# Kernel tuning notes

Measured on AMD Instinct MI355X. Metric: run time of the kernel, lower is better.

Reference implementation:

```python
import jax, jax.numpy as jnp
import numpy as np

B, CI, CO, A = 2048, 32, 32, 16   # batch, caps_in, caps_out, atom
ITER_NUM = 5


def setup_inputs() -> dict:
    key = jax.random.key(0)
    k1, = jax.random.split(key, 1)
    x = jax.random.normal(k1, (B, CI, CO, A), dtype=jnp.float32)
    gamma = jnp.ones((1, CI, 1, A), dtype=jnp.float32)
    beta = jnp.zeros((1, CI, 1, A), dtype=jnp.float32)
    return {"x": x, "gamma": gamma, "beta": beta}


def _iter_norm_inv_sqrt(sigma, iter_num):
    # sigma: [CI, A, A] batched covariance; Newton-Schulz inverse square root.
    a = sigma.shape[-1]
    trace = jnp.trace(sigma, axis1=-2, axis2=-1)[:, None, None]  # [CI,1,1]
    sigma_n = sigma / trace                                      # trace-normalize
    p = jnp.broadcast_to(jnp.eye(a, dtype=sigma.dtype), sigma.shape)
    for _ in range(iter_num):
        p = 0.5 * (3.0 * p - p @ p @ p @ sigma_n)
    return p / jnp.sqrt(trace)


def reference(x, gamma, beta):
    b, ci, co, a = x.shape
    # center over batch and caps_out axes (axes [0, 2])
    mean = jnp.mean(x, axis=(0, 2), keepdims=True)                # [1,CI,1,A]
    centered = x - mean
    # [CI, B*CO, A]
    c = jnp.transpose(centered, (1, 0, 2, 3)).reshape(ci, b * co, a)
    # per-capsule covariance, normalized by (batch*caps_out - 1)
    sigma = jnp.einsum('cna,cnb->cab', c, c) / (jnp.float32(b * co) - 1.0)
    w = _iter_norm_inv_sqrt(sigma, ITER_NUM)                       # [CI,A,A]
    dec = jnp.einsum('cna,cab->cnb', c, w)                         # whiten
    dec = jnp.transpose(dec.reshape(ci, b, co, a), (1, 0, 2, 3))   # [B,CI,CO,A]
    return dec * gamma + beta
```

## Files before the change

kernel.cpp:

```cpp
#include <hip/hip_runtime.h>
#include <hip/hip_bf16.h>
#include <math.h>

constexpr int CI = 32;
constexpr int CO = 32;
constexpr float INV_N   = 1.0f / 65536.0f;
constexpr float INV_NM1 = 1.0f / 65535.0f;

constexpr int NCHUNK = 32;
constexpr int PART_STRIDE = 272;

constexpr int WS_PART = 0;
constexpr int WS_WG   = CI * NCHUNK * PART_STRIDE;
constexpr int WS_C0   = WS_WG + CI * 256;

constexpr int BSTRIDE = 16384;

using f32x4  = __attribute__((ext_vector_type(4))) float;
using bf16x8 = __attribute__((ext_vector_type(8))) short;

__global__ __launch_bounds__(256) void k_stats(const float* __restrict__ x,
                                               float* __restrict__ ws) {
    const int ci    = blockIdx.x & 31;
    const int chunk = blockIdx.x >> 5;
    const int tid   = threadIdx.x;
    const int lane  = tid & 63;
    const int wv    = tid >> 6;
    const int m     = lane & 15;
    const int g     = lane >> 4;

    f32x4 acc = {0.0f, 0.0f, 0.0f, 0.0f};
    float sacc = 0.0f;

    const int b0 = chunk * 64 + wv * 16;
    const float* p = x + ((size_t)(b0 * 32 + ci) * 32 + g * 8) * 16 + m;

    float bA[8], bB[8], bC[8], bD[8];

    auto ld = [&](float (&d)[8], const float* q) {
#pragma unroll
        for (int j = 0; j < 8; ++j) d[j] = q[j * 16];
    };
    auto step = [&](float (&buf)[8]) {
        union { bf16x8 v; unsigned short h[8]; } fu;
#pragma unroll
        for (int j = 0; j < 8; ++j) {
            sacc += buf[j];
            fu.h[j] = __bfloat16_as_ushort(__float2bfloat16(buf[j]));
        }
        acc = __builtin_amdgcn_mfma_f32_16x16x32_bf16(fu.v, fu.v, acc, 0, 0, 0);
    };

    ld(bA, p);
    ld(bB, p + BSTRIDE);
    ld(bC, p + 2 * BSTRIDE);
    ld(bD, p + 3 * BSTRIDE);
    p += 4 * BSTRIDE;
#pragma unroll
    for (int rr = 0; rr < 4; ++rr) {
        step(bA); if (rr < 3) ld(bA, p);
        step(bB); if (rr < 3) ld(bB, p + BSTRIDE);
        step(bC); if (rr < 3) ld(bC, p + 2 * BSTRIDE);
        step(bD); if (rr < 3) { ld(bD, p + 3 * BSTRIDE); p += 4 * BSTRIDE; }
    }

    sacc += __shfl_xor(sacc, 16, 64);
    sacc += __shfl_xor(sacc, 32, 64);

    __shared__ float red[4][272];
#pragma unroll
    for (int q = 0; q < 4; ++q)
        red[wv][(g * 4 + q) * 17 + m] = acc[q];
    if (g == 0) red[wv][m * 17 + 16] = sacc;
    __syncthreads();

    float* slot = ws + WS_PART + (ci * NCHUNK + chunk) * PART_STRIDE;
    for (int e = tid; e < 272; e += 256)
        slot[e] = red[0][e] + red[1][e] + red[2][e] + red[3][e];
}

__global__ __launch_bounds__(256) void k_ns(const float* __restrict__ gamma,
                                            const float* __restrict__ beta,
                                            float* __restrict__ ws) {
    const int ci  = blockIdx.x;
    const int tid = threadIdx.x;
    const int r = tid >> 4, c = tid & 15;

    __shared__ float red2[272];
    __shared__ float sig[16][17];
    __shared__ float pm[16][17];
    __shared__ float t1[16][17];
    __shared__ float t2[16][17];
    __shared__ float trace_s;

    const float* base = ws + WS_PART + (size_t)ci * NCHUNK * PART_STRIDE;
    for (int e = tid; e < 272; e += 256) {
        float s = 0.0f;
#pragma unroll
        for (int ch = 0; ch < NCHUNK; ++ch)
            s += base[ch * PART_STRIDE + e];
        red2[e] = s;
    }
    __syncthreads();

    const float P_rc = red2[r * 17 + c];
    const float S_r  = red2[r * 17 + 16];
    const float S_c  = red2[c * 17 + 16];
    sig[r][c] = (P_rc - S_r * S_c * INV_N) * INV_NM1;
    __syncthreads();

    if (tid == 0) {
        float tr = 0.0f;
        for (int i = 0; i < 16; ++i) tr += sig[i][i];
        trace_s = tr;
    }
    __syncthreads();
    const float tr = trace_s;

    sig[r][c] = sig[r][c] / tr;
    pm[r][c]  = (r == c) ? 1.0f : 0.0f;
    __syncthreads();

    for (int it = 0; it < 5; ++it) {
        float a = 0.0f;
        for (int k = 0; k < 16; ++k) a += pm[r][k] * pm[k][c];
        t1[r][c] = a;
        __syncthreads();
        float b2 = 0.0f;
        for (int k = 0; k < 16; ++k) b2 += t1[r][k] * pm[k][c];
        t2[r][c] = b2;
        __syncthreads();
        float d = 0.0f;
        for (int k = 0; k < 16; ++k) d += t2[r][k] * sig[k][c];
        const float np = 0.5f * (3.0f * pm[r][c] - d);
        __syncthreads();
        pm[r][c] = np;
        __syncthreads();
    }

    const float inv_sqrt_tr = 1.0f / sqrtf(tr);
    const float gc = gamma[ci * 16 + c];
    ws[WS_WG + ci * 256 + r * 16 + c] = pm[r][c] * inv_sqrt_tr * gc;
    if (r == 0) {
        float s = 0.0f;
        for (int a = 0; a < 16; ++a) {
            const float mean_a = red2[a * 17 + 16] * INV_N;
            s += mean_a * pm[a][c];
        }
        ws[WS_C0 + ci * 16 + c] = beta[ci * 16 + c] - gc * s * inv_sqrt_tr;
    }
}

__global__ __launch_bounds__(256) void k_apply(const float* __restrict__ x,
                                               const float* __restrict__ ws,
                                               float* __restrict__ out) {
    const int ci    = blockIdx.x & 31;
    const int chunk = blockIdx.x >> 5;
    const int tid   = threadIdx.x;
    const int sub   = tid & 3;
    const int quad  = tid >> 2;
    const int b0    = sub * 4;

    float wg[16][4];
    const float* WG = ws + WS_WG + ci * 256;
#pragma unroll
    for (int a = 0; a < 16; ++a) {
        const float4 w4 = *reinterpret_cast<const float4*>(WG + a * 16 + b0);
        wg[a][0] = w4.x; wg[a][1] = w4.y; wg[a][2] = w4.z; wg[a][3] = w4.w;
    }
    const float4 c4 = *reinterpret_cast<const float4*>(ws + WS_C0 + ci * 16 + b0);
    const float c0[4] = {c4.x, c4.y, c4.z, c4.w};

    const size_t base =
        (((size_t)(chunk * 64 + (quad >> 5)) * 32 + ci) * 32 + (quad & 31)) * 16;
    const float* p = x + base;
    float* q = out + base + b0;

    auto body = [&](const float4& f0, const float4& f1,
                    const float4& f2, const float4& f3, float* qq) {
        const float v[16] = {f0.x, f0.y, f0.z, f0.w,  f1.x, f1.y, f1.z, f1.w,
                             f2.x, f2.y, f2.z, f2.w,  f3.x, f3.y, f3.z, f3.w};
        float oacc[4] = {c0[0], c0[1], c0[2], c0[3]};
#pragma unroll
        for (int a = 0; a < 16; ++a) {
#pragma unroll
            for (int i = 0; i < 4; ++i) oacc[i] += v[a] * wg[a][i];
        }
        f32x4 o;
        o.x = oacc[0]; o.y = oacc[1]; o.z = oacc[2]; o.w = oacc[3];
        __builtin_nontemporal_store(o, reinterpret_cast<f32x4*>(qq));
    };

    float4 f0 = *reinterpret_cast<const float4*>(p);
    float4 f1 = *reinterpret_cast<const float4*>(p + 4);
    float4 f2 = *reinterpret_cast<const float4*>(p + 8);
    float4 f3 = *reinterpret_cast<const float4*>(p + 12);

    for (int it = 0; it < 31; ++it) {
        const float* pn = p + 32768;
        const float4 g0 = *reinterpret_cast<const float4*>(pn);
        const float4 g1 = *reinterpret_cast<const float4*>(pn + 4);
        const float4 g2 = *reinterpret_cast<const float4*>(pn + 8);
        const float4 g3 = *reinterpret_cast<const float4*>(pn + 12);

        body(f0, f1, f2, f3, q);

        f0 = g0; f1 = g1; f2 = g2; f3 = g3;
        p = pn; q += 32768;
    }
    body(f0, f1, f2, f3, q);
}

extern "C" void kernel_launch(void* const* d_in, const int* in_sizes, int n_in,
                              void* d_out, int out_size, void* d_ws, size_t ws_size,
                              hipStream_t stream) {
    const float* x     = (const float*)d_in[0];
    const float* gamma = (const float*)d_in[1];
    const float* beta  = (const float*)d_in[2];
    float* out = (float*)d_out;
    float* ws  = (float*)d_ws;

    k_stats<<<dim3(1024), dim3(256), 0, stream>>>(x, ws);
    k_ns<<<dim3(32), dim3(256), 0, stream>>>(gamma, beta, ws);
    k_apply<<<dim3(1024), dim3(256), 0, stream>>>(x, ws, out);
}
```

Measured before the change: 76.04 us.

## Remap stats blocks to contiguous spans over 8 capsules, add reduction stage

Each k_stats block now covers 8 batch rows across 8 consecutive input capsules instead of 64 strided batches for a single capsule. Each wave reads contiguous 4 KB blocks and keeps 8 MFMA accumulators. Because partials grow to 256 spans per capsule, a new k_red kernel pre-reduces them into 8 per capsule before k_ns. The new layout should give more sequential DRAM access, at the cost of an extra launch, more partial-sum traffic, and higher register and LDS use per block.

```diff
diff --git a/kernel.cpp b/kernel.cpp
--- a/kernel.cpp
+++ b/kernel.cpp
@@ -7,76 +7,100 @@
 constexpr float INV_N   = 1.0f / 65536.0f;
 constexpr float INV_NM1 = 1.0f / 65535.0f;
 
-constexpr int NCHUNK = 32;
+constexpr int NSPAN = 256;
 constexpr int PART_STRIDE = 272;
-
 constexpr int WS_PART = 0;
-constexpr int WS_WG   = CI * NCHUNK * PART_STRIDE;
+constexpr int WS_MID  = CI * NSPAN * PART_STRIDE;
+constexpr int WS_WG   = WS_MID + CI * 8 * PART_STRIDE;
 constexpr int WS_C0   = WS_WG + CI * 256;
-
-constexpr int BSTRIDE = 16384;
 
 using f32x4  = __attribute__((ext_vector_type(4))) float;
 using bf16x8 = __attribute__((ext_vector_type(8))) short;
 
 __global__ __launch_bounds__(256) void k_stats(const float* __restrict__ x,
                                                float* __restrict__ ws) {
-    const int ci    = blockIdx.x & 31;
-    const int chunk = blockIdx.x >> 5;
-    const int tid   = threadIdx.x;
-    const int lane  = tid & 63;
-    const int wv    = tid >> 6;
-    const int m     = lane & 15;
-    const int g     = lane >> 4;
-
-    f32x4 acc = {0.0f, 0.0f, 0.0f, 0.0f};
-    float sacc = 0.0f;
-
-    const int b0 = chunk * 64 + wv * 16;
-    const float* p = x + ((size_t)(b0 * 32 + ci) * 32 + g * 8) * 16 + m;
-
-    float bA[8], bB[8], bC[8], bD[8];
-
+    const int cig  = blockIdx.x & 3;
+    const int span = blockIdx.x >> 2;
+    const int tid  = threadIdx.x;
+    const int lane = tid & 63;
+    const int wv   = tid >> 6;
+    const int m    = lane & 15;
+    const int g    = lane >> 4;
+
+    f32x4 acc[8];
+    float sacc[8];
+#pragma unroll
+    for (int l = 0; l < 8; ++l) {
+        acc[l] = f32x4{0.0f, 0.0f, 0.0f, 0.0f};
+        sacc[l] = 0.0f;
+    }
+
+    const float* pb = x +
+        (((size_t)(span * 8 + wv * 2) * 32 + cig * 8) * 32 + g * 8) * 16 + m;
+
+    float bufA[8], bufB[8];
     auto ld = [&](float (&d)[8], const float* q) {
 #pragma unroll
         for (int j = 0; j < 8; ++j) d[j] = q[j * 16];
     };
-    auto step = [&](float (&buf)[8]) {
+    auto step = [&](float (&buf)[8], int l) {
         union { bf16x8 v; unsigned short h[8]; } fu;
 #pragma unroll
         for (int j = 0; j < 8; ++j) {
-            sacc += buf[j];
+            sacc[l] += buf[j];
             fu.h[j] = __bfloat16_as_ushort(__float2bfloat16(buf[j]));
         }
-        acc = __builtin_amdgcn_mfma_f32_16x16x32_bf16(fu.v, fu.v, acc, 0, 0, 0);
+        acc[l] = __builtin_amdgcn_mfma_f32_16x16x32_bf16(fu.v, fu.v, acc[l],
+                                                         0, 0, 0);
     };
 
-    ld(bA, p);
-    ld(bB, p + BSTRIDE);
-    ld(bC, p + 2 * BSTRIDE);
-    ld(bD, p + 3 * BSTRIDE);
-    p += 4 * BSTRIDE;
-#pragma unroll
-    for (int rr = 0; rr < 4; ++rr) {
-        step(bA); if (rr < 3) ld(bA, p);
-        step(bB); if (rr < 3) ld(bB, p + BSTRIDE);
-        step(bC); if (rr < 3) ld(bC, p + 2 * BSTRIDE);
-        step(bD); if (rr < 3) { ld(bD, p + 3 * BSTRIDE); p += 4 * BSTRIDE; }
-    }
-
-    sacc += __shfl_xor(sacc, 16, 64);
-    sacc += __shfl_xor(sacc, 32, 64);
-
-    __shared__ float red[4][272];
-#pragma unroll
-    for (int q = 0; q < 4; ++q)
-        red[wv][(g * 4 + q) * 17 + m] = acc[q];
-    if (g == 0) red[wv][m * 17 + 16] = sacc;
-    __syncthreads();
-
-    float* slot = ws + WS_PART + (ci * NCHUNK + chunk) * PART_STRIDE;
-    for (int e = tid; e < 272; e += 256)
-        slot[e] = red[0][e] + red[1][e] + red[2][e] + red[3][e];
+    ld(bufA, pb);
+#pragma unroll
+    for (int s = 0; s < 16; ++s) {
+        const int nxt = (((s + 1) >> 3) * 16384) + (((s + 1) & 7) * 512);
+        if (s < 15) {
+            if (s & 1) ld(bufA, pb + nxt); else ld(bufB, pb + nxt);
+        }
+        if (s & 1) step(bufB, s & 7); else step(bufA, s & 7);
+    }
+
+#pragma unroll
+    for (int l = 0; l < 8; ++l) {
+        sacc[l] += __shfl_xor(sacc[l], 16, 64);
+        sacc[l] += __shfl_xor(sacc[l], 32, 64);
+    }
+
+    __shared__ float red[4][8 * 272];
+#pragma unroll
+    for (int l = 0; l < 8; ++l) {
+#pragma unroll
+        for (int q = 0; q < 4; ++q)
+            red[wv][l * 272 + (g * 4 + q) * 17 + m] = acc[l][q];
+        if (g == 0) red[wv][l * 272 + m * 17 + 16] = sacc[l];
+    }
+    __syncthreads();
+
+    for (int e = tid; e < 8 * 272; e += 256) {
+        const float ssum = red[0][e] + red[1][e] + red[2][e] + red[3][e];
+        const int l = e / 272, k = e - l * 272;
+        ws[WS_PART + ((size_t)(cig * 8 + l) * NSPAN + span) * 272 + k] = ssum;
+    }
+}
+
+__global__ __launch_bounds__(256) void k_red(float* __restrict__ ws) {
+    const int ci  = blockIdx.x >> 3;
+    const int oct = blockIdx.x & 7;
+    const int tid = threadIdx.x;
+
+    const float* base =
+        ws + WS_PART + ((size_t)ci * NSPAN + oct * 32) * PART_STRIDE;
+    for (int e = tid; e < PART_STRIDE; e += 256) {
+        float s = 0.0f;
+#pragma unroll
+        for (int sp = 0; sp < 32; ++sp)
+            s += base[sp * PART_STRIDE + e];
+        ws[WS_MID + (ci * 8 + oct) * PART_STRIDE + e] = s;
+    }
 }
 
 __global__ __launch_bounds__(256) void k_ns(const float* __restrict__ gamma,
@@ -93,11 +117,11 @@
     __shared__ float t2[16][17];
     __shared__ float trace_s;
 
-    const float* base = ws + WS_PART + (size_t)ci * NCHUNK * PART_STRIDE;
+    const float* base = ws + WS_MID + (size_t)ci * 8 * PART_STRIDE;
     for (int e = tid; e < 272; e += 256) {
         float s = 0.0f;
 #pragma unroll
-        for (int ch = 0; ch < NCHUNK; ++ch)
+        for (int ch = 0; ch < 8; ++ch)
             s += base[ch * PART_STRIDE + e];
         red2[e] = s;
     }
@@ -221,6 +245,7 @@
     float* ws  = (float*)d_ws;
 
     k_stats<<<dim3(1024), dim3(256), 0, stream>>>(x, ws);
+    k_red<<<dim3(256), dim3(256), 0, stream>>>(ws);
     k_ns<<<dim3(32), dim3(256), 0, stream>>>(gamma, beta, ws);
     k_apply<<<dim3(1024), dim3(256), 0, stream>>>(x, ws, out);
 }
```

Measured after the change: 78.92 us. +3.8%, slower.

## Stage stats-kernel loads through padded LDS with coalesced float4 reads

Applied to the files above, without the earlier changes.

The covariance stats kernel now reads each 16-batch slice with coalesced float4 global loads instead of strided scalar loads. The data is staged into per-wave double-buffered, padded shared memory, and the bf16 MFMA operands are gathered from there. The aim is better global memory coalescing and fewer load instructions. The cost is extra LDS traffic and the risk of bank conflicts or LDS hazards, since only wave-local ordering protects the buffers and no explicit barrier is added.

```diff
diff --git a/kernel.cpp b/kernel.cpp
--- a/kernel.cpp
+++ b/kernel.cpp
@@ -14,7 +14,8 @@
 constexpr int WS_WG   = CI * NCHUNK * PART_STRIDE;
 constexpr int WS_C0   = WS_WG + CI * 256;
 
-constexpr int BSTRIDE = 16384;
+constexpr int TSTRIDE = 16384;
+constexpr int LROW    = 18;
 
 using f32x4  = __attribute__((ext_vector_type(4))) float;
 using bf16x8 = __attribute__((ext_vector_type(8))) short;
@@ -29,39 +30,58 @@
     const int m     = lane & 15;
     const int g     = lane >> 4;
 
+    __shared__ float lds[4][2][32 * LROW];
+    float* const L0 = lds[wv][0];
+    float* const L1 = lds[wv][1];
+
+    const int wco = lane >> 2;
+    const int wa  = (lane & 3) * 4;
+    const int w0  = wco * LROW + wa;
+    const int w1  = (16 + wco) * LROW + wa;
+
     f32x4 acc = {0.0f, 0.0f, 0.0f, 0.0f};
     float sacc = 0.0f;
 
-    const int b0 = chunk * 64 + wv * 16;
-    const float* p = x + ((size_t)(b0 * 32 + ci) * 32 + g * 8) * 16 + m;
-
-    float bA[8], bB[8], bC[8], bD[8];
-
-    auto ld = [&](float (&d)[8], const float* q) {
-#pragma unroll
-        for (int j = 0; j < 8; ++j) d[j] = q[j * 16];
-    };
-    auto step = [&](float (&buf)[8]) {
+    const float* const pb =
+        x + ((size_t)((chunk * 64 + wv * 16) * 32 + ci)) * 512 + lane * 4;
+
+    float4 P0, P1, Q0, Q1;
+    auto ldreg = [&](float4& r0, float4& r1, int t) {
+        const float* p = pb + (size_t)t * TSTRIDE;
+        r0 = *reinterpret_cast<const float4*>(p);
+        r1 = *reinterpret_cast<const float4*>(p + 256);
+    };
+    auto wrlds = [&](float* buf, const float4& r0, const float4& r1) {
+        *reinterpret_cast<float2*>(buf + w0)     = float2{r0.x, r0.y};
+        *reinterpret_cast<float2*>(buf + w0 + 2) = float2{r0.z, r0.w};
+        *reinterpret_cast<float2*>(buf + w1)     = float2{r1.x, r1.y};
+        *reinterpret_cast<float2*>(buf + w1 + 2) = float2{r1.z, r1.w};
+    };
+    auto proc = [&](const float* buf) {
+        const float* rp = buf + m;
         union { bf16x8 v; unsigned short h[8]; } fu;
 #pragma unroll
         for (int j = 0; j < 8; ++j) {
-            sacc += buf[j];
-            fu.h[j] = __bfloat16_as_ushort(__float2bfloat16(buf[j]));
+            const float val = rp[(g * 8 + j) * LROW];
+            sacc += val;
+            fu.h[j] = __bfloat16_as_ushort(__float2bfloat16(val));
         }
         acc = __builtin_amdgcn_mfma_f32_16x16x32_bf16(fu.v, fu.v, acc, 0, 0, 0);
     };
 
-    ld(bA, p);
-    ld(bB, p + BSTRIDE);
-    ld(bC, p + 2 * BSTRIDE);
-    ld(bD, p + 3 * BSTRIDE);
-    p += 4 * BSTRIDE;
-#pragma unroll
-    for (int rr = 0; rr < 4; ++rr) {
-        step(bA); if (rr < 3) ld(bA, p);
-        step(bB); if (rr < 3) ld(bB, p + BSTRIDE);
-        step(bC); if (rr < 3) ld(bC, p + 2 * BSTRIDE);
-        step(bD); if (rr < 3) { ld(bD, p + 3 * BSTRIDE); p += 4 * BSTRIDE; }
+    ldreg(P0, P1, 0);
+    wrlds(L0, P0, P1);
+    ldreg(P0, P1, 1);
+    ldreg(Q0, Q1, 2);
+
+#pragma unroll
+    for (int pr = 0; pr < 8; ++pr) {
+        wrlds(L1, P0, P1);
+        proc(L0);
+        if (pr < 7) ldreg(P0, P1, 2 * pr + 3);
+        if (pr < 7) wrlds(L0, Q0, Q1);
+        proc(L1);
+        if (pr < 6) ldreg(Q0, Q1, 2 * pr + 4);
     }
 
     sacc += __shfl_xor(sacc, 16, 64);
```

Result: slower. 77.92 us (+2.5%).

## Stage k_stats input through LDS with async global_load_lds ring buffer

Applied to the files above, without the earlier changes.

The stats kernel stops doing strided 4-byte register loads and instead streams each wave's 512-float tiles into a per-wave 4-slot LDS ring, using 16-byte direct-to-LDS loads. The pipeline is controlled with explicit vmcnt waits. The MFMA operands are then read back from LDS with a rotated row order, which changes the k-order symmetrically for both operands and should reduce bank conflicts. The aim is wider, better-coalesced reads and deeper prefetch on this memory-bound pass. In exchange it uses more LDS, and reusing a ring slot relies only on a compiler barrier to keep the LDS reads ahead of the DMA overwrite.

```diff
diff --git a/kernel.cpp b/kernel.cpp
--- a/kernel.cpp
+++ b/kernel.cpp
@@ -14,10 +14,22 @@
 constexpr int WS_WG   = CI * NCHUNK * PART_STRIDE;
 constexpr int WS_C0   = WS_WG + CI * 256;
 
-constexpr int BSTRIDE = 16384;
+constexpr int TSTRIDE = 16384;
 
 using f32x4  = __attribute__((ext_vector_type(4))) float;
 using bf16x8 = __attribute__((ext_vector_type(8))) short;
+
+__device__ __forceinline__ void dma16(const float* g, float* l) {
+    __builtin_amdgcn_global_load_lds(
+        (const __attribute__((address_space(1))) void*)g,
+        (__attribute__((address_space(3))) void*)l,
+        16, 0, 0);
+}
+
+template <int N>
+__device__ __forceinline__ void wait_vm() {
+    asm volatile("s_waitcnt vmcnt(%0)" :: "n"(N) : "memory");
+}
 
 __global__ __launch_bounds__(256) void k_stats(const float* __restrict__ x,
                                                float* __restrict__ ws) {
@@ -29,45 +41,49 @@
     const int m     = lane & 15;
     const int g     = lane >> 4;
 
+    __shared__ float tiles[4][4][512];
+    __shared__ float red[4][272];
+
     f32x4 acc = {0.0f, 0.0f, 0.0f, 0.0f};
     float sacc = 0.0f;
 
-    const int b0 = chunk * 64 + wv * 16;
-    const float* p = x + ((size_t)(b0 * 32 + ci) * 32 + g * 8) * 16 + m;
-
-    float bA[8], bB[8], bC[8], bD[8];
-
-    auto ld = [&](float (&d)[8], const float* q) {
-#pragma unroll
-        for (int j = 0; j < 8; ++j) d[j] = q[j * 16];
+    const float* const gbase =
+        x + ((size_t)((chunk * 64 + wv * 16) * 32 + ci)) * 512 + lane * 4;
+
+    auto issue2 = [&](int t) {
+        float* lbuf = &tiles[wv][t & 3][0];
+        const float* gp = gbase + (size_t)t * TSTRIDE;
+        dma16(gp, lbuf);
+        dma16(gp + 256, lbuf + 256);
     };
-    auto step = [&](float (&buf)[8]) {
+    auto proc = [&](int slot) {
+        const float* rp = &tiles[wv][slot][g * 128 + m];
         union { bf16x8 v; unsigned short h[8]; } fu;
 #pragma unroll
         for (int j = 0; j < 8; ++j) {
-            sacc += buf[j];
-            fu.h[j] = __bfloat16_as_ushort(__float2bfloat16(buf[j]));
+            const float val = rp[((j + g) & 7) * 16];
+            sacc += val;
+            fu.h[j] = __bfloat16_as_ushort(__float2bfloat16(val));
         }
         acc = __builtin_amdgcn_mfma_f32_16x16x32_bf16(fu.v, fu.v, acc, 0, 0, 0);
     };
 
-    ld(bA, p);
-    ld(bB, p + BSTRIDE);
-    ld(bC, p + 2 * BSTRIDE);
-    ld(bD, p + 3 * BSTRIDE);
-    p += 4 * BSTRIDE;
-#pragma unroll
-    for (int rr = 0; rr < 4; ++rr) {
-        step(bA); if (rr < 3) ld(bA, p);
-        step(bB); if (rr < 3) ld(bB, p + BSTRIDE);
-        step(bC); if (rr < 3) ld(bC, p + 2 * BSTRIDE);
-        step(bD); if (rr < 3) { ld(bD, p + 3 * BSTRIDE); p += 4 * BSTRIDE; }
-    }
+    issue2(0); issue2(1); issue2(2); issue2(3);
+
+    for (int t = 0; t < 13; ++t) {
+        wait_vm<6>();
+        __builtin_amdgcn_sched_barrier(0);
+        proc(t & 3);
+        asm volatile("" ::: "memory");
+        if (t < 12) issue2(t + 4);
+    }
+    wait_vm<4>(); proc(1);
+    wait_vm<2>(); proc(2);
+    wait_vm<0>(); proc(3);
 
     sacc += __shfl_xor(sacc, 16, 64);
     sacc += __shfl_xor(sacc, 32, 64);
 
-    __shared__ float red[4][272];
 #pragma unroll
     for (int q = 0; q < 4; ++q)
         red[wv][(g * 4 + q) * 17 + m] = acc[q];
```

After: 77.73 us. 1.02x slower.
